# Kernel tuning notes

Hardware: AMD Instinct MI355X
Metric: run time of the kernel (lower is better)

## Reference

```python
import jax, jax.numpy as jnp
import numpy as np

B, S, D, H = 4, 2048, 1024, 16
DH = D // H
SCALE = 1.0 / np.sqrt(DH).astype(np.float32)


def setup_inputs() -> dict:
    key = jax.random.key(0)
    k1, k2, k3 = jax.random.split(key, 3)
    x = jax.random.normal(k1, (B, S, D), dtype=jnp.float32)
    w_qkv = jax.random.normal(k2, (D, 3 * D), dtype=jnp.float32) * (1.0 / np.sqrt(D))
    b_qkv = jnp.zeros((3 * D,), dtype=jnp.float32)
    w_out = jax.random.normal(k3, (D, D), dtype=jnp.float32) * (1.0 / np.sqrt(D))
    b_out = jnp.zeros((D,), dtype=jnp.float32)
    return {"x": x, "w_qkv": w_qkv, "b_qkv": b_qkv, "w_out": w_out, "b_out": b_out}


def reference(x, w_qkv, b_qkv, w_out, b_out):
    b, s, d = x.shape
    qkv = x @ w_qkv + b_qkv                       # [b, s, 3d]
    qkv = qkv.reshape(b, s, 3, H, DH)
    qkv = jnp.transpose(qkv, (2, 0, 3, 1, 4))     # [3, b, h, s, dh]
    q, k, v = qkv[0], qkv[1], qkv[2]
    scores = jnp.einsum("bhqd,bhkd->bhqk", q, k) * SCALE
    weights = jax.nn.softmax(scores, axis=-1)
    attn = jnp.einsum("bhqk,bhkd->bhqd", weights, v)
    attn = jnp.transpose(attn, (0, 2, 1, 3)).reshape(b, s, d)
    return attn @ w_out + b_out
```

## Files before the change

### kernel.cpp

```cpp
#include <hip/hip_runtime.h>


typedef _Float16 f16;
typedef __attribute__((ext_vector_type(8))) _Float16 f16x8;
typedef __attribute__((ext_vector_type(4))) _Float16 f16x4;
typedef __attribute__((ext_vector_type(4))) float f32x4;
typedef __attribute__((ext_vector_type(16))) float f32x16;
typedef __attribute__((ext_vector_type(4))) unsigned u32x4;
typedef __attribute__((ext_vector_type(2))) int i32x2;

#define MFMA16F(a, b, c) __builtin_amdgcn_mfma_f32_16x16x32_f16((a), (b), (c), 0, 0, 0)
#define MFMA32F(a, b, c) __builtin_amdgcn_mfma_f32_32x32x16_f16((a), (b), (c), 0, 0, 0)

__device__ __forceinline__ i32x2 pl32_swap(unsigned a, unsigned b) {
  return __builtin_amdgcn_permlane32_swap((int)a, (int)b, false, false);
}

__device__ __forceinline__ void gload16(void* lds, const void* g) {
  __builtin_amdgcn_global_load_lds(
      (const __attribute__((address_space(1))) unsigned int*)g,
      (__attribute__((address_space(3))) unsigned int*)lds, 16, 0, 0);
}

__device__ __forceinline__ f16* lds_addr(f16* t, int row, int col) {
  return (f16*)((char*)t + row * 128 + ((col * 2) ^ ((row & 7) << 4)));
}
__device__ __forceinline__ f16x8 lds8(const f16* t, int row, int col) {
  return *(const f16x8*)lds_addr((f16*)t, row, col);
}

#define Q_PRESCALE 0.18033688011117f

__global__ __launch_bounds__(256) void cast_kernel(const float* __restrict__ in,
                                                   f16* __restrict__ out, int n) {
  int idx = (blockIdx.x * 256 + threadIdx.x) * 8;
  const int stride = gridDim.x * 256 * 8;
  for (; idx < n; idx += stride) {
    float v[8];
    *(float4*)&v[0] = *(const float4*)&in[idx];
    *(float4*)&v[4] = *(const float4*)&in[idx + 4];
    f16x8 h;
#pragma unroll
    for (int j = 0; j < 8; ++j) h[j] = (f16)v[j];
    *(f16x8*)&out[idx] = h;
  }
}

__global__ __launch_bounds__(256) void transpose_h_kernel(
    const float* __restrict__ in, f16* __restrict__ t_hi, int R, int C) {
  __shared__ float tile[64][65];
  const int r0 = blockIdx.y * 64;
  const int c0 = blockIdx.x * 64;
  const int tid = threadIdx.x;
  const int lr = tid >> 4;
  const int lc = (tid & 15) * 4;
#pragma unroll
  for (int i = 0; i < 4; ++i) {
    float4 v = *(const float4*)&in[(size_t)(r0 + lr + i * 16) * C + c0 + lc];
    tile[lr + i * 16][lc] = v.x;
    tile[lr + i * 16][lc + 1] = v.y;
    tile[lr + i * 16][lc + 2] = v.z;
    tile[lr + i * 16][lc + 3] = v.w;
  }
  __syncthreads();
#pragma unroll
  for (int p = 0; p < 2; ++p) {
    const int id = p * 256 + tid;
    const int oc = id >> 3;
    const int orr = (id & 7) * 8;
    f16x8 h;
#pragma unroll
    for (int j = 0; j < 8; ++j) h[j] = (f16)tile[orr + j][oc];
    *(f16x8*)&t_hi[(size_t)(c0 + oc) * R + r0 + orr] = h;
  }
}

template <int MODE>
__global__ __launch_bounds__(256, 2) void gemm_kernel(
    const f16* __restrict__ A, const f16* __restrict__ BT,
    const float* __restrict__ bias,
    f16* __restrict__ q_h, f16* __restrict__ k_h, f16* __restrict__ vt_h,
    float* __restrict__ C, int M, int N, int K) {
  __shared__ __align__(16) f16 As[2][128 * 64];
  __shared__ __align__(16) f16 Bs[2][128 * 64];

  const int tid = threadIdx.x;
  const int lane = tid & 63;
  const int wv = tid >> 6;
  const int lo16 = lane & 15;
  const int hi4 = lane >> 4;
  const int wr = wv >> 1;
  const int wc = wv & 1;
  const int m0 = blockIdx.y * 128;
  const int n0 = blockIdx.x * 128;

  f32x4 acc[4][4];
#pragma unroll
  for (int i = 0; i < 4; ++i)
#pragma unroll
    for (int j = 0; j < 4; ++j) acc[i][j] = (f32x4){0.f, 0.f, 0.f, 0.f};

  auto stage = [&](int buf, int kt) {
#pragma unroll
    for (int p = 0; p < 4; ++p) {
      const int cbase = p * 256 + wv * 64;
      const int c = cbase + lane;
      const int row = c >> 3;
      const int colc = (c & 7) ^ (row & 7);
      gload16(&As[buf][cbase * 8], &A[(size_t)(m0 + row) * K + kt + colc * 8]);
      gload16(&Bs[buf][cbase * 8], &BT[(size_t)(n0 + row) * K + kt + colc * 8]);
    }
  };

  stage(0, 0);
  __syncthreads();

  const int NT = K >> 6;
  int cur = 0;
  for (int t = 0; t < NT; ++t) {
    if (t + 1 < NT) stage(cur ^ 1, (t + 1) * 64);
    const f16* Ac = As[cur];
    const f16* Bc = Bs[cur];
#pragma unroll
    for (int ks = 0; ks < 2; ++ks) {
      f16x8 ah[4], bh[4];
#pragma unroll
      for (int t4 = 0; t4 < 4; ++t4) {
        ah[t4] = lds8((f16*)Ac, wr * 64 + t4 * 16 + lo16, ks * 32 + hi4 * 8);
        bh[t4] = lds8((f16*)Bc, wc * 64 + t4 * 16 + lo16, ks * 32 + hi4 * 8);
      }
#pragma unroll
      for (int mt = 0; mt < 4; ++mt)
#pragma unroll
        for (int nt = 0; nt < 4; ++nt)
          acc[mt][nt] = MFMA16F(ah[mt], bh[nt], acc[mt][nt]);
    }
    __syncthreads();
    cur ^= 1;
  }

#pragma unroll
  for (int mt = 0; mt < 4; ++mt) {
    const int gmb = m0 + wr * 64 + mt * 16 + hi4 * 4;
#pragma unroll
    for (int nt = 0; nt < 4; ++nt) {
      const int gn = n0 + wc * 64 + nt * 16 + lo16;
      float v[4];
#pragma unroll
      for (int r = 0; r < 4; ++r) v[r] = acc[mt][nt][r] + bias[gn];
      if (MODE == 0) {
#pragma unroll
        for (int r = 0; r < 4; ++r) C[(size_t)(gmb + r) * N + gn] = v[r];
      } else {
        const int which = gn >> 10;
        const int h = (gn >> 6) & 15;
        const int dh = gn & 63;
        const int b = gmb >> 11;
        const int s = gmb & 2047;
        const size_t bh = (size_t)b * 16 + h;
        if (which == 0) {
#pragma unroll
          for (int r = 0; r < 4; ++r)
            q_h[(bh * 2048 + s + r) * 64 + dh] = (f16)(v[r] * Q_PRESCALE);
        } else if (which == 1) {
#pragma unroll
          for (int r = 0; r < 4; ++r)
            k_h[(bh * 2048 + s + r) * 64 + dh] = (f16)v[r];
        } else {
          f16x4 hh;
#pragma unroll
          for (int r = 0; r < 4; ++r) hh[r] = (f16)v[r];
          *(f16x4*)&vt_h[(bh * 64 + dh) * 2048 + s] = hh;
        }
      }
    }
  }
}

__global__ __launch_bounds__(256, 4) void attn_kernel(
    const f16* __restrict__ q_h, const f16* __restrict__ k_h,
    const f16* __restrict__ vt_h, f16* __restrict__ o) {
  __shared__ __align__(16) f16 Kh[2][64 * 64], Vh[2][64 * 64];
  __shared__ float Ls[4][32];

  const int tid = threadIdx.x;
  const int lane = tid & 63;
  const int wv = tid >> 6;
  const int l31 = lane & 31;
  const int h2 = lane >> 5;
  const int id0 = blockIdx.x;
  const int id = ((id0 & 7) << 7) | (id0 >> 3);
  const int bh = id >> 4;
  const int qb = id & 15;
  const size_t kvbase = (size_t)bh * 2048 * 64;
  const size_t vtbase = (size_t)bh * 64 * 2048;
  const int q0 = qb * 128 + wv * 32;

  const int c0idx = wv * 64 + lane;
  const int srow = c0idx >> 3;
  const int scol = ((c0idx & 7) ^ (srow & 7)) * 8;
  const int c1idx = 256 + wv * 64 + lane;
  const int srow1 = c1idx >> 3;
  const int scol1 = ((c1idx & 7) ^ (srow1 & 7)) * 8;

  auto stage = [&](int buf, int kv0) {
    gload16(&Kh[buf][(wv * 64) * 8], &k_h[kvbase + (size_t)(kv0 + srow) * 64 + scol]);
    gload16(&Vh[buf][(wv * 64) * 8], &vt_h[vtbase + (size_t)srow * 2048 + kv0 + scol]);
    gload16(&Kh[buf][(256 + wv * 64) * 8], &k_h[kvbase + (size_t)(kv0 + srow1) * 64 + scol1]);
    gload16(&Vh[buf][(256 + wv * 64) * 8], &vt_h[vtbase + (size_t)srow1 * 2048 + kv0 + scol1]);
  };

  f16x8 qh[4];
#pragma unroll
  for (int kt = 0; kt < 4; ++kt)
    qh[kt] = *(const f16x8*)&q_h[kvbase + (size_t)(q0 + l31) * 64 + kt * 16 + h2 * 8];

  float lp = 0.f;
  f32x16 o_acc[2];
#pragma unroll
  for (int i = 0; i < 16; ++i) {
    o_acc[0][i] = 0.f;
    o_acc[1][i] = 0.f;
  }

  stage(0, 0);
  __syncthreads();

  int cur = 0;
  for (int t = 0; t < 32; ++t) {
    if (t + 1 < 32) stage(cur ^ 1, (t + 1) * 64);
    const f16* Kc = Kh[cur];
    const f16* Vc = Vh[cur];

#pragma unroll
    for (int s = 0; s < 2; ++s) {
      f32x16 sa;
#pragma unroll
      for (int i = 0; i < 16; ++i) sa[i] = 0.f;
#pragma unroll
      for (int kt = 0; kt < 4; ++kt) {
        f16x8 kb = lds8((f16*)Kc, s * 32 + l31, kt * 16 + h2 * 8);
        sa = MFMA32F(kb, qh[kt], sa);
      }

      unsigned w[8];
#pragma unroll
      for (int m = 0; m < 8; ++m) {
        const float pa_f = __builtin_amdgcn_exp2f(sa[2 * m]);
        const float pb_f = __builtin_amdgcn_exp2f(sa[2 * m + 1]);
        lp += pa_f + pb_f;
        auto pk = __builtin_amdgcn_cvt_pkrtz(pa_f, pb_f);
        w[m] = __builtin_bit_cast(unsigned, pk);
      }

      f16x8 pa[2];
#pragma unroll
      for (int b = 0; b < 2; ++b) {
        const i32x2 r02 = pl32_swap(w[4 * b + 0], w[4 * b + 2]);
        const i32x2 r13 = pl32_swap(w[4 * b + 1], w[4 * b + 3]);
        u32x4 tw;
        tw[0] = (unsigned)r02[0];
        tw[1] = (unsigned)r13[0];
        tw[2] = (unsigned)r02[1];
        tw[3] = (unsigned)r13[1];
        pa[b] = __builtin_bit_cast(f16x8, tw);
      }

#pragma unroll
      for (int dt = 0; dt < 2; ++dt)
#pragma unroll
        for (int b = 0; b < 2; ++b) {
          f16x8 vb = lds8((f16*)Vc, dt * 32 + l31, s * 32 + b * 16 + h2 * 8);
          o_acc[dt] = MFMA32F(pa[b], vb, o_acc[dt]);
        }
    }
    __syncthreads();
    cur ^= 1;
  }

  lp += __shfl_xor(lp, 32);
  Ls[wv][l31] = 1.0f / lp;
  float linv[16];
#pragma unroll
  for (int r = 0; r < 16; ++r) linv[r] = Ls[wv][(r & 3) + 8 * (r >> 2) + 4 * h2];

  const int b_ = bh >> 4;
  const int h_ = bh & 15;
#pragma unroll
  for (int dt = 0; dt < 2; ++dt)
#pragma unroll
    for (int r = 0; r < 16; ++r) {
      const int s_row = q0 + (r & 3) + 8 * (r >> 2) + 4 * h2;
      const size_t idx =
          ((size_t)(b_ * 2048 + s_row)) * 1024 + h_ * 64 + dt * 32 + l31;
      o[idx] = (f16)(o_acc[dt][r] * linv[r]);
    }
}

extern "C" void kernel_launch(void* const* d_in, const int* in_sizes, int n_in,
                              void* d_out, int out_size, void* d_ws, size_t ws_size,
                              hipStream_t stream) {
  const float* x = (const float*)d_in[0];
  const float* w_qkv = (const float*)d_in[1];
  const float* b_qkv = (const float*)d_in[2];
  const float* w_out = (const float*)d_in[3];
  const float* b_out = (const float*)d_in[4];
  float* out = (float*)d_out;

  f16* ws = (f16*)d_ws;
  const size_t SZ = (size_t)64 * 2048 * 64;
  f16* q_h = ws;
  f16* k_h = ws + SZ;
  f16* vt_h = ws + 2 * SZ;
  f16* x_h = ws + 3 * SZ;
  f16* wqT_h = ws + 4 * SZ;
  f16* woT_h = wqT_h + (size_t)3072 * 1024;

  dim3 blk(256);
  cast_kernel<<<dim3(4096), blk, 0, stream>>>(x, x_h, 8 * 1024 * 1024);
  transpose_h_kernel<<<dim3(48, 16), blk, 0, stream>>>(w_qkv, wqT_h, 1024, 3072);
  transpose_h_kernel<<<dim3(16, 16), blk, 0, stream>>>(w_out, woT_h, 1024, 1024);

  gemm_kernel<1><<<dim3(24, 64), blk, 0, stream>>>(
      x_h, wqT_h, b_qkv, q_h, k_h, vt_h, nullptr, 8192, 3072, 1024);

  attn_kernel<<<dim3(1024), blk, 0, stream>>>(q_h, k_h, vt_h, x_h);

  gemm_kernel<0><<<dim3(8, 64), blk, 0, stream>>>(
      x_h, woT_h, b_out, nullptr, nullptr, nullptr, out, 8192, 1024, 1024);
}
```

Before: 194.6 us.

## Compute softmax row sums via MFMA with ones, unroll double buffer, add setprio

The attention kernel now builds the softmax denominator with an extra MFMA of the probability tile against a ones vector. This replaces the per-lane scalar adds, cross-lane shuffle and LDS round trip for the row-sum reciprocal. Both the GEMM and attention main loops are unrolled by two with fixed buffer indices instead of a toggled cur index. MFMA sections are wrapped in s_setprio raises to favour matrix issue. The extra MFMA adds matrix work per tile, and the row sums now come from f16-rounded probabilities rather than fp32 values.

```diff
diff --git a/kernel.cpp b/kernel.cpp
--- a/kernel.cpp
+++ b/kernel.cpp
@@ -112,15 +112,7 @@
     }
   };
 
-  stage(0, 0);
-  __syncthreads();
-
-  const int NT = K >> 6;
-  int cur = 0;
-  for (int t = 0; t < NT; ++t) {
-    if (t + 1 < NT) stage(cur ^ 1, (t + 1) * 64);
-    const f16* Ac = As[cur];
-    const f16* Bc = Bs[cur];
+  auto compute = [&](const f16* Ac, const f16* Bc) {
 #pragma unroll
     for (int ks = 0; ks < 2; ++ks) {
       f16x8 ah[4], bh[4];
@@ -129,14 +121,27 @@
         ah[t4] = lds8((f16*)Ac, wr * 64 + t4 * 16 + lo16, ks * 32 + hi4 * 8);
         bh[t4] = lds8((f16*)Bc, wc * 64 + t4 * 16 + lo16, ks * 32 + hi4 * 8);
       }
+      __builtin_amdgcn_s_setprio(1);
 #pragma unroll
       for (int mt = 0; mt < 4; ++mt)
 #pragma unroll
         for (int nt = 0; nt < 4; ++nt)
           acc[mt][nt] = MFMA16F(ah[mt], bh[nt], acc[mt][nt]);
-    }
+      __builtin_amdgcn_s_setprio(0);
+    }
+  };
+
+  stage(0, 0);
+  __syncthreads();
+
+  const int NT = K >> 6;
+  for (int t = 0; t < NT; t += 2) {
+    if (t + 1 < NT) stage(1, (t + 1) * 64);
+    compute(As[0], Bs[0]);
     __syncthreads();
-    cur ^= 1;
+    if (t + 2 < NT) stage(0, (t + 2) * 64);
+    compute(As[1], Bs[1]);
+    __syncthreads();
   }
 
 #pragma unroll
@@ -181,7 +186,6 @@
     const f16* __restrict__ q_h, const f16* __restrict__ k_h,
     const f16* __restrict__ vt_h, f16* __restrict__ o) {
   __shared__ __align__(16) f16 Kh[2][64 * 64], Vh[2][64 * 64];
-  __shared__ float Ls[4][32];
 
   const int tid = threadIdx.x;
   const int lane = tid & 63;
@@ -215,40 +219,35 @@
   for (int kt = 0; kt < 4; ++kt)
     qh[kt] = *(const f16x8*)&q_h[kvbase + (size_t)(q0 + l31) * 64 + kt * 16 + h2 * 8];
 
-  float lp = 0.f;
-  f32x16 o_acc[2];
+  const f16x8 ones = {(f16)1, (f16)1, (f16)1, (f16)1, (f16)1, (f16)1, (f16)1, (f16)1};
+
+  f32x16 o_acc[2], acc_l;
 #pragma unroll
   for (int i = 0; i < 16; ++i) {
     o_acc[0][i] = 0.f;
     o_acc[1][i] = 0.f;
-  }
-
-  stage(0, 0);
-  __syncthreads();
-
-  int cur = 0;
-  for (int t = 0; t < 32; ++t) {
-    if (t + 1 < 32) stage(cur ^ 1, (t + 1) * 64);
-    const f16* Kc = Kh[cur];
-    const f16* Vc = Vh[cur];
-
+    acc_l[i] = 0.f;
+  }
+
+  auto tile_compute = [&](const f16* Kc, const f16* Vc) {
 #pragma unroll
     for (int s = 0; s < 2; ++s) {
       f32x16 sa;
 #pragma unroll
       for (int i = 0; i < 16; ++i) sa[i] = 0.f;
+      __builtin_amdgcn_s_setprio(1);
 #pragma unroll
       for (int kt = 0; kt < 4; ++kt) {
         f16x8 kb = lds8((f16*)Kc, s * 32 + l31, kt * 16 + h2 * 8);
         sa = MFMA32F(kb, qh[kt], sa);
       }
+      __builtin_amdgcn_s_setprio(0);
 
       unsigned w[8];
 #pragma unroll
       for (int m = 0; m < 8; ++m) {
         const float pa_f = __builtin_amdgcn_exp2f(sa[2 * m]);
         const float pb_f = __builtin_amdgcn_exp2f(sa[2 * m + 1]);
-        lp += pa_f + pb_f;
         auto pk = __builtin_amdgcn_cvt_pkrtz(pa_f, pb_f);
         w[m] = __builtin_bit_cast(unsigned, pk);
       }
@@ -266,23 +265,31 @@
         pa[b] = __builtin_bit_cast(f16x8, tw);
       }
 
-#pragma unroll
-      for (int dt = 0; dt < 2; ++dt)
-#pragma unroll
-        for (int b = 0; b < 2; ++b) {
+      __builtin_amdgcn_s_setprio(1);
+#pragma unroll
+      for (int b = 0; b < 2; ++b) {
+        acc_l = MFMA32F(pa[b], ones, acc_l);
+#pragma unroll
+        for (int dt = 0; dt < 2; ++dt) {
           f16x8 vb = lds8((f16*)Vc, dt * 32 + l31, s * 32 + b * 16 + h2 * 8);
           o_acc[dt] = MFMA32F(pa[b], vb, o_acc[dt]);
         }
-    }
+      }
+      __builtin_amdgcn_s_setprio(0);
+    }
+  };
+
+  stage(0, 0);
+  __syncthreads();
+
+  for (int t = 0; t < 32; t += 2) {
+    if (t + 1 < 32) stage(1, (t + 1) * 64);
+    tile_compute(Kh[0], Vh[0]);
     __syncthreads();
-    cur ^= 1;
-  }
-
-  lp += __shfl_xor(lp, 32);
-  Ls[wv][l31] = 1.0f / lp;
-  float linv[16];
-#pragma unroll
-  for (int r = 0; r < 16; ++r) linv[r] = Ls[wv][(r & 3) + 8 * (r >> 2) + 4 * h2];
+    if (t + 2 < 32) stage(0, (t + 2) * 64);
+    tile_compute(Kh[1], Vh[1]);
+    __syncthreads();
+  }
 
   const int b_ = bh >> 4;
   const int h_ = bh & 15;
@@ -293,7 +300,7 @@
       const int s_row = q0 + (r & 3) + 8 * (r >> 2) + 4 * h2;
       const size_t idx =
           ((size_t)(b_ * 2048 + s_row)) * 1024 + h_ * 64 + dt * 32 + l31;
-      o[idx] = (f16)(o_acc[dt][r] * linv[r]);
+      o[idx] = (f16)(o_acc[dt][r] / acc_l[r]);
     }
 }
 
```

After: 193.1 us. No clear change (-0.8%).
